# Kernel optimization log

Hardware: AMD Instinct MI355X
Metric: run time of the kernel (lower is better)

## Reference

```python
import jax, jax.numpy as jnp
import numpy as np

N = 100000   # nodes
E = 1600000  # edges (avg degree 16)
D = 128      # input feature dim d
H = 128      # args.hidden_channels


def setup_inputs() -> dict:
    key = jax.random.key(0)
    ks = jax.random.split(key, 20)
    def lin(k, fi, fo):
        return jax.random.normal(k, (fi, fo), jnp.float32) / np.sqrt(fi).astype(np.float32)
    inp = {
        'x': jax.random.normal(ks[0], (N, D), jnp.float32),
        'edge_index': jax.random.randint(ks[1], (2, E), 0, N, dtype=jnp.int32),
        # ir_Learner GCN (d -> h -> h)
        'W_ir1': lin(ks[2], D, H), 'b_ir1': jnp.zeros((H,), jnp.float32),
        'W_ir2': lin(ks[3], H, H), 'b_ir2': jnp.zeros((H,), jnp.float32),
        # main gnn GCN (d -> h -> h)
        'W_g1': lin(ks[4], D, H), 'b_g1': jnp.zeros((H,), jnp.float32),
        'W_g2': lin(ks[5], H, H), 'b_g2': jnp.zeros((H,), jnp.float32),
        # decoder GCN (2h -> h -> d) + LayerNorm(d)
        'W_d1': lin(ks[6], 2 * H, H), 'b_d1': jnp.zeros((H,), jnp.float32),
        'W_d2': lin(ks[7], H, D), 'b_d2': jnp.zeros((D,), jnp.float32),
        'ln_g': jnp.ones((D,), jnp.float32), 'ln_b': jnp.zeros((D,), jnp.float32),
        'step': 3,
    }
    return inp


def _gcn_edges(edge_index, n):
    # add self loops, symmetric normalization D^-1/2 (A+I) D^-1/2
    loop = jnp.arange(n, dtype=edge_index.dtype)
    src = jnp.concatenate([edge_index[0], loop])
    dst = jnp.concatenate([edge_index[1], loop])
    deg = jax.ops.segment_sum(jnp.ones_like(dst, jnp.float32), dst, num_segments=n)
    dis = jax.lax.rsqrt(jnp.maximum(deg, 1.0))
    coef = dis[src] * dis[dst]  # [E+N]
    return src, dst, coef


def _conv(x, W, b, src, dst, coef, n):
    h = x @ W                                   # linear first (PyG GCNConv)
    agg = jax.ops.segment_sum(h[src] * coef[:, None], dst, num_segments=n)
    return agg + b


def _gcn2(x, W1, b1, W2, b2, src, dst, coef, n):
    h = jax.nn.relu(_conv(x, W1, b1, src, dst, coef, n))
    return _conv(h, W2, b2, src, dst, coef, n)


def _linear_cka(X, Y):
    # feature-space equivalent of Gram-matrix linear CKA (avoids NxN)
    Xc = X - jnp.mean(X, axis=0, keepdims=True)
    Yc = Y - jnp.mean(Y, axis=0, keepdims=True)
    hsic = jnp.sum((Xc.T @ Yc) ** 2)
    nx = jnp.sqrt(jnp.sum((Xc.T @ Xc) ** 2))
    ny = jnp.sqrt(jnp.sum((Yc.T @ Yc) ** 2))
    return hsic / (nx * ny)


def reference(x, edge_index, W_ir1, b_ir1, W_ir2, b_ir2, W_g1, b_g1, W_g2, b_g2,
              W_d1, b_d1, W_d2, b_d2, ln_g, ln_b, step):
    n = x.shape[0]
    src, dst, coef = _gcn_edges(edge_index, n)
    # step == 3 path
    env = jnp.tanh(_gcn2(x, W_ir1, b_ir1, W_ir2, b_ir2, src, dst, coef, n))   # ir_Learner
    inv = _gcn2(x, W_g1, b_g1, W_g2, b_g2, src, dst, coef, n)                 # main gnn
    dec = _gcn2(jnp.concatenate([env, inv], axis=1), W_d1, b_d1, W_d2, b_d2,
                src, dst, coef, n)                                            # decoder GCN
    mu = jnp.mean(dec, axis=-1, keepdims=True)
    var = jnp.mean((dec - mu) ** 2, axis=-1, keepdims=True)
    rebuilt = (dec - mu) * jax.lax.rsqrt(var + 1e-5) * ln_g + ln_b            # LayerNorm
    ind_loss = _linear_cka(env, inv)                                          # HSIC, kernel='linear', idp_type='xo'
    return ind_loss, rebuilt
```

## Files before the change

### kernel.cpp

```cpp
#include <hip/hip_runtime.h>
#include <hip/hip_bf16.h>


#define HD 128

__global__ void k_deg(const int* __restrict__ dst, int* __restrict__ degi, int E) {
  int i = blockIdx.x * blockDim.x + threadIdx.x;
  if (i < E) atomicAdd(&degi[dst[i]], 1);
}

__global__ void k_dis(const int* __restrict__ degi, float* __restrict__ dis, int n) {
  int i = blockIdx.x * blockDim.x + threadIdx.x;
  if (i < n) dis[i] = rsqrtf((float)degi[i] + 1.0f);
}

__global__ __launch_bounds__(1024) void k_scan(const int* __restrict__ degi,
    int* __restrict__ row_ptr, int* __restrict__ cursor, int N) {
  __shared__ int s[1024];
  const int tid = threadIdx.x;
  const int chunk = (N + 1023) / 1024;
  const int beg = tid * chunk;
  const int end = min(beg + chunk, N);
  int sum = 0;
  for (int i = beg; i < end; ++i) sum += degi[i];
  s[tid] = sum;
  __syncthreads();
  for (int off = 1; off < 1024; off <<= 1) {
    int v = (tid >= off) ? s[tid - off] : 0;
    __syncthreads();
    s[tid] += v;
    __syncthreads();
  }
  int run = s[tid] - sum;
  for (int i = beg; i < end; ++i) {
    row_ptr[i] = run;
    cursor[i] = run;
    run += degi[i];
  }
  if (tid == 1023) row_ptr[N] = s[1023];
}

__global__ void k_fill(const int* __restrict__ src, const int* __restrict__ dst,
    const float* __restrict__ dis, int* __restrict__ cursor,
    int* __restrict__ csr_src, float* __restrict__ csr_coef, int E) {
  int e = blockIdx.x * blockDim.x + threadIdx.x;
  if (e >= E) return;
  int s = src[e], d = dst[e];
  int pos = atomicAdd(&cursor[d], 1);
  csr_src[pos] = s;
  csr_coef[pos] = dis[s] * dis[d];
}

template<int K>
__global__ __launch_bounds__(256) void k_gemm(const float* __restrict__ X1,
    const float* __restrict__ X2, const float* __restrict__ W,
    float* __restrict__ C, int n) {
  __shared__ float Ws[64 * 128];
  __shared__ float Xs[32 * 64];
  const int tid = threadIdx.x;
  const int row0 = blockIdx.x * 32;
  const int rg = tid >> 5;
  const int c0 = (tid & 31) * 4;
  float acc[4][4] = {};
  for (int kc = 0; kc < K; kc += 64) {
    const float* Xp = (kc < 128) ? X1 : X2;
    const int kof = (kc < 128) ? kc : kc - 128;
    __syncthreads();
    {
      const float4* Wg = (const float4*)(W + (size_t)kc * 128);
      float4* Wl = (float4*)Ws;
      for (int v = tid; v < 64 * 128 / 4; v += 256) Wl[v] = Wg[v];
    }
    for (int v = tid; v < 32 * 64 / 4; v += 256) {
      int r = v >> 4, k4 = v & 15;
      int rr = row0 + r; if (rr > n - 1) rr = n - 1;
      ((float4*)(Xs + r * 64))[k4] =
          ((const float4*)(Xp + (size_t)rr * 128 + kof))[k4];
    }
    __syncthreads();
#pragma unroll
    for (int k4 = 0; k4 < 64; k4 += 4) {
      float4 xv[4];
#pragma unroll
      for (int i = 0; i < 4; ++i)
        xv[i] = *(const float4*)(Xs + (rg + 8 * i) * 64 + k4);
#pragma unroll
      for (int kk = 0; kk < 4; ++kk) {
        float4 w = *(const float4*)(Ws + (k4 + kk) * 128 + c0);
#pragma unroll
        for (int i = 0; i < 4; ++i) {
          float x = ((const float*)&xv[i])[kk];
          acc[i][0] = fmaf(x, w.x, acc[i][0]);
          acc[i][1] = fmaf(x, w.y, acc[i][1]);
          acc[i][2] = fmaf(x, w.z, acc[i][2]);
          acc[i][3] = fmaf(x, w.w, acc[i][3]);
        }
      }
    }
  }
#pragma unroll
  for (int i = 0; i < 4; ++i) {
    int r = row0 + rg + 8 * i;
    if (r < n) {
      float4 o = { acc[i][0], acc[i][1], acc[i][2], acc[i][3] };
      *(float4*)(C + (size_t)r * 128 + c0) = o;
    }
  }
}

__global__ __launch_bounds__(256) void k_gather(const float* __restrict__ h,
    const int* __restrict__ row_ptr, const int* __restrict__ csr_src,
    const float* __restrict__ csr_coef, const float* __restrict__ dis,
    const float* __restrict__ bias, float* __restrict__ out,
    const float* __restrict__ lng, const float* __restrict__ lnb,
    float* __restrict__ lnout, int act, int N) {
  int node = blockIdx.x * 4 + (threadIdx.x >> 6);
  if (node >= N) return;
  int lane = threadIdx.x & 63;
  int beg = row_ptr[node], end = row_ptr[node + 1];
  float ax = 0.f, ay = 0.f;
  int j = beg;
  for (; j + 2 <= end; j += 2) {
    int s0 = csr_src[j], s1 = csr_src[j + 1];
    float c0 = csr_coef[j], c1 = csr_coef[j + 1];
    float2 h0 = *(const float2*)(h + (size_t)s0 * HD + lane * 2);
    float2 h1 = *(const float2*)(h + (size_t)s1 * HD + lane * 2);
    ax = fmaf(h0.x, c0, ax); ay = fmaf(h0.y, c0, ay);
    ax = fmaf(h1.x, c1, ax); ay = fmaf(h1.y, c1, ay);
  }
  if (j < end) {
    int s0 = csr_src[j];
    float c0 = csr_coef[j];
    float2 h0 = *(const float2*)(h + (size_t)s0 * HD + lane * 2);
    ax = fmaf(h0.x, c0, ax); ay = fmaf(h0.y, c0, ay);
  }
  float sc = dis[node]; sc *= sc;
  float2 hd = *(const float2*)(h + (size_t)node * HD + lane * 2);
  float2 bv = *(const float2*)(bias + lane * 2);
  float vx = fmaf(hd.x, sc, ax) + bv.x;
  float vy = fmaf(hd.y, sc, ay) + bv.y;
  if (act == 1) { vx = fmaxf(vx, 0.f); vy = fmaxf(vy, 0.f); }
  else if (act == 2) { vx = tanhf(vx); vy = tanhf(vy); }
  if (act != 3) {
    float2 o = { vx, vy };
    *(float2*)(out + (size_t)node * HD + lane * 2) = o;
  } else {
    float s = vx + vy;
    for (int o = 32; o; o >>= 1) s += __shfl_xor(s, o);
    float mu = s * (1.0f / HD);
    float dx = vx - mu, dy = vy - mu;
    float q = fmaf(dx, dx, dy * dy);
    for (int o = 32; o; o >>= 1) q += __shfl_xor(q, o);
    float rs = rsqrtf(q * (1.0f / HD) + 1e-5f);
    float2 gv = *(const float2*)(lng + lane * 2);
    float2 lb = *(const float2*)(lnb + lane * 2);
    size_t o0 = (size_t)node * HD + (size_t)lane * 2;
    lnout[o0]     = fmaf(dx * rs, gv.x, lb.x);
    lnout[o0 + 1] = fmaf(dy * rs, gv.y, lb.y);
  }
}

__global__ void k_colsum(const float* __restrict__ A, const float* __restrict__ B,
                         float* __restrict__ sums, int N) {
  int col = threadIdx.x & 127;
  int sel = threadIdx.x >> 7;
  const float* P = sel ? B : A;
  float s = 0.f;
  for (int r = blockIdx.x; r < N; r += gridDim.x)
    s += P[(size_t)r * HD + col];
  atomicAdd(&sums[sel * HD + col], s);
}

__global__ __launch_bounds__(256) void k_gram(const float* __restrict__ env,
    const float* __restrict__ inv, const float* __restrict__ sums,
    float* __restrict__ G, int N) {
  const int g = blockIdx.y;
  const float* X = (g == 1) ? inv : env;
  const float* Y = (g == 0) ? env : inv;
  const float* mxs = sums + ((g == 1) ? HD : 0);
  const float* mys = sums + ((g == 0) ? 0 : HD);
  __shared__ float Xs[8 * HD], Ys[8 * HD];
  __shared__ float mux[HD], muy[HD];
  const int tid = threadIdx.x;
  if (tid < HD) mux[tid] = mxs[tid] * (1.0f / N);
  else muy[tid - HD] = mys[tid - HD] * (1.0f / N);
  const int i0 = (tid >> 4) * 8;
  const int j0 = (tid & 15) * 8;
  float acc[8][8] = {};
  __syncthreads();
  for (int r0 = blockIdx.x * 8; r0 < N; r0 += gridDim.x * 8) {
    __syncthreads();
    for (int t = tid; t < 8 * HD; t += 256) {
      int rr = t >> 7, cc = t & 127;
      int r = r0 + rr;
      float xv = 0.f, yv = 0.f;
      if (r < N) {
        xv = X[(size_t)r * HD + cc] - mux[cc];
        yv = Y[(size_t)r * HD + cc] - muy[cc];
      }
      Xs[rr * HD + cc] = xv;
      Ys[rr * HD + cc] = yv;
    }
    __syncthreads();
#pragma unroll
    for (int rr = 0; rr < 8; ++rr) {
      float4 xa = *(const float4*)(Xs + rr * HD + i0);
      float4 xb = *(const float4*)(Xs + rr * HD + i0 + 4);
      float4 ya = *(const float4*)(Ys + rr * HD + j0);
      float4 yb = *(const float4*)(Ys + rr * HD + j0 + 4);
      float xv[8] = {xa.x, xa.y, xa.z, xa.w, xb.x, xb.y, xb.z, xb.w};
      float yv[8] = {ya.x, ya.y, ya.z, ya.w, yb.x, yb.y, yb.z, yb.w};
#pragma unroll
      for (int i = 0; i < 8; ++i)
#pragma unroll
        for (int j = 0; j < 8; ++j)
          acc[i][j] = fmaf(xv[i], yv[j], acc[i][j]);
    }
  }
  float* Gp = G + (size_t)g * HD * HD;
#pragma unroll
  for (int i = 0; i < 8; ++i)
#pragma unroll
    for (int j = 0; j < 8; ++j)
      atomicAdd(&Gp[(size_t)(i0 + i) * HD + (j0 + j)], acc[i][j]);
}

__global__ void k_cka(const float* __restrict__ G, float* __restrict__ out0) {
  float sxx = 0.f, syy = 0.f, sxy = 0.f;
  for (int i = threadIdx.x; i < HD * HD; i += 256) {
    float a = G[i];               sxx = fmaf(a, a, sxx);
    float b = G[HD * HD + i];     syy = fmaf(b, b, syy);
    float c = G[2 * HD * HD + i]; sxy = fmaf(c, c, sxy);
  }
  for (int o = 32; o; o >>= 1) {
    sxx += __shfl_down(sxx, o);
    syy += __shfl_down(syy, o);
    sxy += __shfl_down(sxy, o);
  }
  __shared__ float red[3][4];
  int wave = threadIdx.x >> 6, lane = threadIdx.x & 63;
  if (lane == 0) { red[0][wave] = sxx; red[1][wave] = syy; red[2][wave] = sxy; }
  __syncthreads();
  if (threadIdx.x == 0) {
    float xx = red[0][0] + red[0][1] + red[0][2] + red[0][3];
    float yy = red[1][0] + red[1][1] + red[1][2] + red[1][3];
    float xy = red[2][0] + red[2][1] + red[2][2] + red[2][3];
    out0[0] = xy / (sqrtf(xx) * sqrtf(yy));
  }
}

extern "C" void kernel_launch(void* const* d_in, const int* in_sizes, int n_in,
                              void* d_out, int out_size, void* d_ws, size_t ws_size,
                              hipStream_t stream) {
  const float* x     = (const float*)d_in[0];
  const int*   ei    = (const int*)d_in[1];
  const float* W_ir1 = (const float*)d_in[2];
  const float* b_ir1 = (const float*)d_in[3];
  const float* W_ir2 = (const float*)d_in[4];
  const float* b_ir2 = (const float*)d_in[5];
  const float* W_g1  = (const float*)d_in[6];
  const float* b_g1  = (const float*)d_in[7];
  const float* W_g2  = (const float*)d_in[8];
  const float* b_g2  = (const float*)d_in[9];
  const float* W_d1  = (const float*)d_in[10];
  const float* b_d1  = (const float*)d_in[11];
  const float* W_d2  = (const float*)d_in[12];
  const float* b_d2  = (const float*)d_in[13];
  const float* ln_g  = (const float*)d_in[14];
  const float* ln_b  = (const float*)d_in[15];

  const int N = in_sizes[0] / HD;
  const int E = in_sizes[1] / 2;
  const int* src = ei;
  const int* dst = ei + E;
  float* out = (float*)d_out;

  const size_t NH = (size_t)N * HD;
  char* w = (char*)d_ws;
  float* A       = (float*)w; w += NH * sizeof(float);
  float* B       = (float*)w; w += NH * sizeof(float);
  float* H       = (float*)w; w += NH * sizeof(float);
  float* dis     = (float*)w; w += (size_t)N * sizeof(float);
  int*   degi    = (int*)w;   w += (size_t)N * sizeof(int);
  int*   row_ptr = (int*)w;   w += ((size_t)N + 4) * sizeof(int);
  int*   cursor  = (int*)w;   w += (size_t)N * sizeof(int);
  int*   csr_src = (int*)w;   w += (size_t)E * sizeof(int);
  float* csr_cf  = (float*)w; w += (size_t)E * sizeof(float);
  float* sums    = (float*)w; w += 256 * sizeof(float);
  float* G       = (float*)w;

  hipMemsetAsync(degi, 0, (size_t)N * sizeof(int), stream);
  k_deg<<<(E + 255) / 256, 256, 0, stream>>>(dst, degi, E);
  k_dis<<<(N + 255) / 256, 256, 0, stream>>>(degi, dis, N);
  k_scan<<<1, 1024, 0, stream>>>(degi, row_ptr, cursor, N);
  k_fill<<<(E + 255) / 256, 256, 0, stream>>>(src, dst, dis, cursor,
                                              csr_src, csr_cf, E);

  const int gblocks = (N + 31) / 32;
  const int ablocks = (N + 3) / 4;

  auto conv = [&](const float* X1, const float* X2, int K, const float* Wm,
                  const float* bias, float* res, int act) {
    if (K == 128) k_gemm<128><<<gblocks, 256, 0, stream>>>(X1, X2, Wm, H, N);
    else          k_gemm<256><<<gblocks, 256, 0, stream>>>(X1, X2, Wm, H, N);
    k_gather<<<ablocks, 256, 0, stream>>>(H, row_ptr, csr_src, csr_cf, dis,
                                          bias, res, ln_g, ln_b, out + 1, act, N);
  };

  conv(x, nullptr, 128, W_ir1, b_ir1, A, 1);
  conv(A, nullptr, 128, W_ir2, b_ir2, A, 2);
  conv(x, nullptr, 128, W_g1, b_g1, B, 1);
  conv(B, nullptr, 128, W_g2, b_g2, B, 0);

  hipMemsetAsync(sums, 0, 256 * sizeof(float), stream);
  hipMemsetAsync(G, 0, 3 * HD * HD * sizeof(float), stream);
  k_colsum<<<512, 256, 0, stream>>>(A, B, sums, N);
  dim3 gg(256, 3);
  k_gram<<<gg, 256, 0, stream>>>(A, B, sums, G, N);
  k_cka<<<1, 256, 0, stream>>>(G, out);

  conv(A, B, 256, W_d1, b_d1, A, 1);
  conv(A, nullptr, 128, W_d2, b_d2, nullptr, 3);
}
```

Baseline: 2.255 ms.

## Move CKA mean-centering into final correction and widen gram tiles

The Gram kernel now accumulates raw X^T Y and the mean correction (N·mu_x·mu_y^T) is subtracted in the final CKA kernel. This removes per-element centering from the hot loop. The Gram loop also stages 16 rows per iteration using vectorized float4 loads into padded, permuted shared memory to reduce bank conflicts, and the grid is doubled. The gather loop is unrolled by 4 to put more loads in flight. Using uncentered accumulation risks precision loss through cancellation in fp32 when means are large.

```diff
diff --git a/kernel.cpp b/kernel.cpp
--- a/kernel.cpp
+++ b/kernel.cpp
@@ -3,6 +3,9 @@
 
 
 #define HD 128
+#define RS 144
+
+__device__ __forceinline__ int gperm(int g) { return g * 8 + ((g >> 2) << 2); }
 
 __global__ void k_deg(const int* __restrict__ dst, int* __restrict__ degi, int E) {
   int i = blockIdx.x * blockDim.x + threadIdx.x;
@@ -120,15 +123,21 @@
   int beg = row_ptr[node], end = row_ptr[node + 1];
   float ax = 0.f, ay = 0.f;
   int j = beg;
-  for (; j + 2 <= end; j += 2) {
+  for (; j + 4 <= end; j += 4) {
     int s0 = csr_src[j], s1 = csr_src[j + 1];
+    int s2 = csr_src[j + 2], s3 = csr_src[j + 3];
     float c0 = csr_coef[j], c1 = csr_coef[j + 1];
+    float c2 = csr_coef[j + 2], c3 = csr_coef[j + 3];
     float2 h0 = *(const float2*)(h + (size_t)s0 * HD + lane * 2);
     float2 h1 = *(const float2*)(h + (size_t)s1 * HD + lane * 2);
+    float2 h2 = *(const float2*)(h + (size_t)s2 * HD + lane * 2);
+    float2 h3 = *(const float2*)(h + (size_t)s3 * HD + lane * 2);
     ax = fmaf(h0.x, c0, ax); ay = fmaf(h0.y, c0, ay);
     ax = fmaf(h1.x, c1, ax); ay = fmaf(h1.y, c1, ay);
-  }
-  if (j < end) {
+    ax = fmaf(h2.x, c2, ax); ay = fmaf(h2.y, c2, ay);
+    ax = fmaf(h3.x, c3, ax); ay = fmaf(h3.y, c3, ay);
+  }
+  for (; j < end; ++j) {
     int s0 = csr_src[j];
     float c0 = csr_coef[j];
     float2 h0 = *(const float2*)(h + (size_t)s0 * HD + lane * 2);
@@ -172,44 +181,45 @@
 }
 
 __global__ __launch_bounds__(256) void k_gram(const float* __restrict__ env,
-    const float* __restrict__ inv, const float* __restrict__ sums,
-    float* __restrict__ G, int N) {
+    const float* __restrict__ inv, float* __restrict__ G, int N) {
   const int g = blockIdx.y;
   const float* X = (g == 1) ? inv : env;
   const float* Y = (g == 0) ? env : inv;
-  const float* mxs = sums + ((g == 1) ? HD : 0);
-  const float* mys = sums + ((g == 0) ? 0 : HD);
-  __shared__ float Xs[8 * HD], Ys[8 * HD];
-  __shared__ float mux[HD], muy[HD];
+  __shared__ float Xs[16 * RS], Ys[16 * RS];
   const int tid = threadIdx.x;
-  if (tid < HD) mux[tid] = mxs[tid] * (1.0f / N);
-  else muy[tid - HD] = mys[tid - HD] * (1.0f / N);
-  const int i0 = (tid >> 4) * 8;
-  const int j0 = (tid & 15) * 8;
+  const int gi = tid >> 4;
+  const int gj = tid & 15;
+  const int xb = gperm(gi), yb = gperm(gj);
+  const int rr_ = tid >> 4;
+  const int sg  = tid & 15;
+  const int soff = rr_ * RS + gperm(sg);
+  const int gcol = sg * 8;
   float acc[8][8] = {};
-  __syncthreads();
-  for (int r0 = blockIdx.x * 8; r0 < N; r0 += gridDim.x * 8) {
-    __syncthreads();
-    for (int t = tid; t < 8 * HD; t += 256) {
-      int rr = t >> 7, cc = t & 127;
-      int r = r0 + rr;
-      float xv = 0.f, yv = 0.f;
+  for (int r0 = blockIdx.x * 16; r0 < N; r0 += gridDim.x * 16) {
+    __syncthreads();
+    {
+      int r = r0 + rr_;
+      float4 x0 = {0,0,0,0}, x1 = x0, y0 = x0, y1 = x0;
       if (r < N) {
-        xv = X[(size_t)r * HD + cc] - mux[cc];
-        yv = Y[(size_t)r * HD + cc] - muy[cc];
+        const float* xp = X + (size_t)r * HD + gcol;
+        const float* yp = Y + (size_t)r * HD + gcol;
+        x0 = ((const float4*)xp)[0]; x1 = ((const float4*)xp)[1];
+        y0 = ((const float4*)yp)[0]; y1 = ((const float4*)yp)[1];
       }
-      Xs[rr * HD + cc] = xv;
-      Ys[rr * HD + cc] = yv;
-    }
-    __syncthreads();
-#pragma unroll
-    for (int rr = 0; rr < 8; ++rr) {
-      float4 xa = *(const float4*)(Xs + rr * HD + i0);
-      float4 xb = *(const float4*)(Xs + rr * HD + i0 + 4);
-      float4 ya = *(const float4*)(Ys + rr * HD + j0);
-      float4 yb = *(const float4*)(Ys + rr * HD + j0 + 4);
-      float xv[8] = {xa.x, xa.y, xa.z, xa.w, xb.x, xb.y, xb.z, xb.w};
-      float yv[8] = {ya.x, ya.y, ya.z, ya.w, yb.x, yb.y, yb.z, yb.w};
+      *(float4*)(Xs + soff)     = x0;
+      *(float4*)(Xs + soff + 4) = x1;
+      *(float4*)(Ys + soff)     = y0;
+      *(float4*)(Ys + soff + 4) = y1;
+    }
+    __syncthreads();
+#pragma unroll
+    for (int rr = 0; rr < 16; ++rr) {
+      float4 xa = *(const float4*)(Xs + rr * RS + xb);
+      float4 xc = *(const float4*)(Xs + rr * RS + xb + 4);
+      float4 ya = *(const float4*)(Ys + rr * RS + yb);
+      float4 yc = *(const float4*)(Ys + rr * RS + yb + 4);
+      float xv[8] = {xa.x, xa.y, xa.z, xa.w, xc.x, xc.y, xc.z, xc.w};
+      float yv[8] = {ya.x, ya.y, ya.z, ya.w, yc.x, yc.y, yc.z, yc.w};
 #pragma unroll
       for (int i = 0; i < 8; ++i)
 #pragma unroll
@@ -222,15 +232,25 @@
   for (int i = 0; i < 8; ++i)
 #pragma unroll
     for (int j = 0; j < 8; ++j)
-      atomicAdd(&Gp[(size_t)(i0 + i) * HD + (j0 + j)], acc[i][j]);
-}
-
-__global__ void k_cka(const float* __restrict__ G, float* __restrict__ out0) {
+      atomicAdd(&Gp[(size_t)(gi * 8 + i) * HD + (gj * 8 + j)], acc[i][j]);
+}
+
+__global__ void k_cka(const float* __restrict__ G, const float* __restrict__ sums,
+                      float* __restrict__ out0, float Nf) {
+  __shared__ float muA[HD], muB[HD];
+  const int tid = threadIdx.x;
+  if (tid < HD) muA[tid] = sums[tid] * (1.0f / Nf);
+  else          muB[tid - HD] = sums[tid] * (1.0f / Nf);
+  __syncthreads();
   float sxx = 0.f, syy = 0.f, sxy = 0.f;
-  for (int i = threadIdx.x; i < HD * HD; i += 256) {
-    float a = G[i];               sxx = fmaf(a, a, sxx);
-    float b = G[HD * HD + i];     syy = fmaf(b, b, syy);
-    float c = G[2 * HD * HD + i]; sxy = fmaf(c, c, sxy);
+  for (int i = tid; i < HD * HD; i += 256) {
+    int r = i >> 7, c = i & 127;
+    float a = G[i]               - Nf * muA[r] * muA[c];
+    float b = G[HD * HD + i]     - Nf * muB[r] * muB[c];
+    float d = G[2 * HD * HD + i] - Nf * muA[r] * muB[c];
+    sxx = fmaf(a, a, sxx);
+    syy = fmaf(b, b, syy);
+    sxy = fmaf(d, d, sxy);
   }
   for (int o = 32; o; o >>= 1) {
     sxx += __shfl_down(sxx, o);
@@ -238,10 +258,10 @@
     sxy += __shfl_down(sxy, o);
   }
   __shared__ float red[3][4];
-  int wave = threadIdx.x >> 6, lane = threadIdx.x & 63;
+  int wave = tid >> 6, lane = tid & 63;
   if (lane == 0) { red[0][wave] = sxx; red[1][wave] = syy; red[2][wave] = sxy; }
   __syncthreads();
-  if (threadIdx.x == 0) {
+  if (tid == 0) {
     float xx = red[0][0] + red[0][1] + red[0][2] + red[0][3];
     float yy = red[1][0] + red[1][1] + red[1][2] + red[1][3];
     float xy = red[2][0] + red[2][1] + red[2][2] + red[2][3];
@@ -315,9 +335,9 @@
   hipMemsetAsync(sums, 0, 256 * sizeof(float), stream);
   hipMemsetAsync(G, 0, 3 * HD * HD * sizeof(float), stream);
   k_colsum<<<512, 256, 0, stream>>>(A, B, sums, N);
-  dim3 gg(256, 3);
-  k_gram<<<gg, 256, 0, stream>>>(A, B, sums, G, N);
-  k_cka<<<1, 256, 0, stream>>>(G, out);
+  dim3 gg(512, 3);
+  k_gram<<<gg, 256, 0, stream>>>(A, B, G, N);
+  k_cka<<<1, 256, 0, stream>>>(G, sums, out, (float)N);
 
   conv(A, B, 256, W_d1, b_d1, A, 1);
   conv(A, nullptr, 128, W_d2, b_d2, nullptr, 3);
```

Result: slower. 2.584 ms (+14.6%).
